# Performance work log

Measured on AMD Instinct MI355X. Metric: run time of the kernel, lower is better.

## Reference

```python
import jax, jax.numpy as jnp
import numpy as np

T, D, H = 2048, 2048, 16
C = D // H  # head dim = 128

def setup_inputs() -> dict:
    key = jax.random.key(0)
    k1, k2, k3 = jax.random.split(key, 3)
    x = jax.random.normal(k1, (T, D), dtype=jnp.float32)
    W_attn = jax.random.normal(k2, (3 * D, D), dtype=jnp.float32) * 0.02
    W_proj = jax.random.normal(k3, (D, D), dtype=jnp.float32) * 0.02
    return {"x": x, "W_attn": W_attn, "W_proj": W_proj}

def reference(x, W_attn, W_proj):
    # c_attn: per-token Linear -> [T, 3D]
    qkv = x @ W_attn.T
    q, k, v = jnp.split(qkv, 3, axis=-1)  # each [T, D]
    # [T, D] -> [H, T, C]
    q = q.reshape(T, H, C).transpose(1, 0, 2)
    k = k.reshape(T, H, C).transpose(1, 0, 2)
    v = v.reshape(T, H, C).transpose(1, 0, 2)
    # raw scores [H, T, T]
    scores = jnp.einsum('htc,hsc->hts', q, k)
    causal_mask = jnp.tril(jnp.ones((1, T, T))) == 0
    scores = jnp.where(causal_mask, float('-inf'), scores)
    orig_dtype = scores.dtype
    # NOTE: original scales AFTER masking, inside softmax, in fp32
    attn = jax.nn.softmax(scores.astype(jnp.float32) / jnp.sqrt(jnp.float32(C)), axis=-1)
    attn = attn.astype(orig_dtype)
    out = attn @ v  # [H, T, C]
    out = out.transpose(1, 0, 2).reshape(T, D)
    return out @ W_proj.T
```

## Files before the change

### kernel.cpp

```cpp
#include <hip/hip_runtime.h>
#include <hip/hip_bf16.h>
#include <stdint.h>

typedef __attribute__((ext_vector_type(8))) __bf16 bf16x8;
typedef __attribute__((ext_vector_type(4))) float f32x4;
typedef __attribute__((ext_vector_type(4))) unsigned int u32x4;
typedef __attribute__((ext_vector_type(4))) unsigned short u16x4;

__device__ __forceinline__ unsigned short f2bf(float f) {
  union { float f; unsigned int u; } v; v.f = f;
  unsigned int r = v.u + 0x7fffu + ((v.u >> 16) & 1u);
  return (unsigned short)(r >> 16);
}

__device__ __forceinline__ void gload_lds16(const void* g, void* l) {
  __builtin_amdgcn_global_load_lds(
      (const __attribute__((address_space(1))) unsigned int*)g,
      (__attribute__((address_space(3))) unsigned int*)l, 16, 0, 0);
}

__global__ __launch_bounds__(256) void cast_f32_bf16(const float* __restrict__ in,
                                                     unsigned short* __restrict__ out,
                                                     int n) {
  int i = (blockIdx.x * 256 + threadIdx.x) * 4;
  if (i >= n) return;
  f32x4 v = *(const f32x4*)&in[i];
  u16x4 o;
  o[0] = f2bf(v[0]); o[1] = f2bf(v[1]); o[2] = f2bf(v[2]); o[3] = f2bf(v[3]);
  *(u16x4*)&out[i] = o;
}

__global__ __launch_bounds__(256) void addf32(float* __restrict__ out,
                                              const float* __restrict__ part, int n) {
  int i = (blockIdx.x * 256 + threadIdx.x) * 4;
  if (i >= n) return;
  f32x4 a = *(const f32x4*)&out[i];
  f32x4 b = *(const f32x4*)&part[i];
  a[0] += b[0]; a[1] += b[1]; a[2] += b[2]; a[3] += b[3];
  *(f32x4*)&out[i] = a;
}

template<int OUT_BF16>
__global__ __launch_bounds__(256) void gemm_bt(const unsigned short* __restrict__ A,
                                               const unsigned short* __restrict__ B,
                                               void* __restrict__ Cv,
                                               float* __restrict__ Cp,
                                               int M, int N, int K, int KS) {
  __shared__ unsigned short As[2][128 * 32];
  __shared__ unsigned short Bs[2][128 * 32];

  const int tid  = threadIdx.x;
  const int lane = tid & 63;
  const int wave = tid >> 6;
  const int wr = (wave >> 1) * 64;
  const int wc = (wave & 1) * 64;
  const int row0 = blockIdx.y * 128;
  const int col0 = blockIdx.x * 128;
  const int l16 = lane & 15;
  const int lk  = (lane >> 4) * 8;
  const int kbeg = blockIdx.z * KS;

  const int srow = lane >> 2;
  const int sc   = (lane & 3) * 8;

  f32x4 acc[4][4] = {};

#pragma unroll
  for (int i = 0; i < 2; ++i) {
    int t = wave * 2 + i;
    int r = t * 16 + srow;
    gload_lds16(&A[(size_t)(row0 + r) * K + kbeg + sc], &As[0][t * 512]);
    gload_lds16(&B[(size_t)(col0 + r) * K + kbeg + sc], &Bs[0][t * 512]);
  }
  __syncthreads();

  int cur = 0;
  for (int k0 = kbeg; k0 < kbeg + KS; k0 += 32, cur ^= 1) {
    if (k0 + 32 < kbeg + KS) {
#pragma unroll
      for (int i = 0; i < 2; ++i) {
        int t = wave * 2 + i;
        int r = t * 16 + srow;
        gload_lds16(&A[(size_t)(row0 + r) * K + k0 + 32 + sc], &As[cur ^ 1][t * 512]);
        gload_lds16(&B[(size_t)(col0 + r) * K + k0 + 32 + sc], &Bs[cur ^ 1][t * 512]);
      }
    }

    bf16x8 af[4], bfr[4];
#pragma unroll
    for (int i = 0; i < 4; ++i) af[i]  = *(const bf16x8*)&As[cur][(wr + i * 16 + l16) * 32 + lk];
#pragma unroll
    for (int i = 0; i < 4; ++i) bfr[i] = *(const bf16x8*)&Bs[cur][(wc + i * 16 + l16) * 32 + lk];
#pragma unroll
    for (int i = 0; i < 4; ++i)
#pragma unroll
      for (int j = 0; j < 4; ++j)
        acc[i][j] = __builtin_amdgcn_mfma_f32_16x16x32_bf16(af[i], bfr[j], acc[i][j], 0, 0, 0);

    __syncthreads();
  }

  void* outp = (blockIdx.z == 0) ? Cv : (void*)Cp;

  const int orow = (lane >> 4) * 4;
#pragma unroll
  for (int i = 0; i < 4; ++i)
#pragma unroll
    for (int j = 0; j < 4; ++j)
#pragma unroll
      for (int r = 0; r < 4; ++r) {
        size_t gr = row0 + wr + i * 16 + orow + r;
        size_t gc = col0 + wc + j * 16 + l16;
        float v = acc[i][j][r];
        if (OUT_BF16) ((unsigned short*)outp)[gr * N + gc] = f2bf(v);
        else          ((float*)outp)[gr * N + gc] = v;
      }
}

#define KS_IDX(r, c) ((((r) * 128) + (c)) ^ (((r) & 7) << 3))
#define VT_IDX(c, t) ((((c) * 64) + (t)) ^ (((((c) ^ ((c) >> 3))) & 7) << 3))
#define PS_IDX(q, c) ((((q) * 64) + (c)) ^ (((((q) & 7) ^ (((q) >> 2) & 3))) << 3))

__global__ __launch_bounds__(256, 2) void attn_kernel(const unsigned short* __restrict__ qkv,
                                                      unsigned short* __restrict__ ctx) {
  __shared__ unsigned short Ks[2][64 * 128];
  __shared__ unsigned short VTs[2][128 * 64];
  __shared__ unsigned short Ps[4][16 * 64];

  const int tid  = threadIdx.x;
  const int lane = tid & 63;
  const int w    = tid >> 6;
  const int l16  = lane & 15;
  const int lk8  = (lane >> 4) * 8;

  const int flat = blockIdx.x + blockIdx.y * 32;
  int h, qb;
  if (flat < 256) { h = flat >> 5; qb = flat & 31; }
  else            { int f2 = flat - 256; h = 8 + (f2 >> 5); qb = 31 - (f2 & 31); }

  const int qrow = qb * 64 + w * 16;

  const unsigned short* Kbase = qkv + 2048 + h * 128;
  const unsigned short* Vbase = qkv + 4096 + h * 128;

  bf16x8 qf[4];
#pragma unroll
  for (int kk = 0; kk < 4; ++kk)
    qf[kk] = *(const bf16x8*)&qkv[(size_t)(qrow + l16) * 6144 + h * 128 + kk * 32 + lk8];

  f32x4 o[8] = {};
  float m[4], ls[4];
#pragma unroll
  for (int r = 0; r < 4; ++r) { m[r] = -1e30f; ls[r] = 0.f; }

  const float sscale = 0.08838834764831845f * 1.4426950408889634f;
  const int qg0 = qrow + (lane >> 4) * 4;

  const int t0v = (tid & 15) * 4;
  const int c0v = (tid >> 4) * 8;

  {
    u32x4 kr[4], vr[4];
#pragma unroll
    for (int it = 0; it < 4; ++it) {
      int idx = it * 256 + tid;
      int row = idx >> 4, c0 = (idx & 15) * 8;
      kr[it] = *(const u32x4*)&Kbase[(size_t)row * 6144 + c0];
    }
#pragma unroll
    for (int r = 0; r < 4; ++r)
      vr[r] = *(const u32x4*)&Vbase[(size_t)(t0v + r) * 6144 + c0v];
#pragma unroll
    for (int it = 0; it < 4; ++it) {
      int idx = it * 256 + tid;
      int row = idx >> 4, c0 = (idx & 15) * 8;
      *(u32x4*)&Ks[0][KS_IDX(row, c0)] = kr[it];
    }
    const unsigned short* p0 = (const unsigned short*)&vr[0];
    const unsigned short* p1 = (const unsigned short*)&vr[1];
    const unsigned short* p2 = (const unsigned short*)&vr[2];
    const unsigned short* p3 = (const unsigned short*)&vr[3];
#pragma unroll
    for (int j = 0; j < 8; ++j) {
      u16x4 wv; wv[0] = p0[j]; wv[1] = p1[j]; wv[2] = p2[j]; wv[3] = p3[j];
      *(u16x4*)&VTs[0][VT_IDX(c0v + j, t0v)] = wv;
    }
  }

  const int nkb = qb + 1;
  for (int kb = 0; kb < nkb; ++kb) {
    const int cur = kb & 1;
    const bool pre = (kb + 1 < nkb);

    u32x4 kr[4], vr[4];
    if (pre) {
#pragma unroll
      for (int it = 0; it < 4; ++it) {
        int idx = it * 256 + tid;
        int row = idx >> 4, c0 = (idx & 15) * 8;
        kr[it] = *(const u32x4*)&Kbase[(size_t)((kb + 1) * 64 + row) * 6144 + c0];
      }
#pragma unroll
      for (int r = 0; r < 4; ++r)
        vr[r] = *(const u32x4*)&Vbase[(size_t)((kb + 1) * 64 + t0v + r) * 6144 + c0v];
    }

    __syncthreads();

    if (pre) {
#pragma unroll
      for (int it = 0; it < 4; ++it) {
        int idx = it * 256 + tid;
        int row = idx >> 4, c0 = (idx & 15) * 8;
        *(u32x4*)&Ks[cur ^ 1][KS_IDX(row, c0)] = kr[it];
      }
      const unsigned short* p0 = (const unsigned short*)&vr[0];
      const unsigned short* p1 = (const unsigned short*)&vr[1];
      const unsigned short* p2 = (const unsigned short*)&vr[2];
      const unsigned short* p3 = (const unsigned short*)&vr[3];
#pragma unroll
      for (int j = 0; j < 8; ++j) {
        u16x4 wv; wv[0] = p0[j]; wv[1] = p1[j]; wv[2] = p2[j]; wv[3] = p3[j];
        *(u16x4*)&VTs[cur ^ 1][VT_IDX(c0v + j, t0v)] = wv;
      }
    }

    f32x4 s[4] = {};
#pragma unroll
    for (int n = 0; n < 4; ++n)
#pragma unroll
      for (int kk = 0; kk < 4; ++kk) {
        bf16x8 kf = *(const bf16x8*)&Ks[cur][KS_IDX(n * 16 + l16, kk * 32 + lk8)];
        s[n] = __builtin_amdgcn_mfma_f32_16x16x32_bf16(qf[kk], kf, s[n], 0, 0, 0);
      }

    const bool diag = (kb == qb);
    float pmax[4];
#pragma unroll
    for (int r = 0; r < 4; ++r) pmax[r] = -1e30f;
#pragma unroll
    for (int n = 0; n < 4; ++n) {
      int kg = kb * 64 + n * 16 + l16;
#pragma unroll
      for (int r = 0; r < 4; ++r) {
        float v = s[n][r] * sscale;
        if (diag && kg > qg0 + r) v = -1e30f;
        s[n][r] = v;
        pmax[r] = fmaxf(pmax[r], v);
      }
    }

    bool need = (pmax[0] > m[0] + 8.f) | (pmax[1] > m[1] + 8.f) |
                (pmax[2] > m[2] + 8.f) | (pmax[3] > m[3] + 8.f);
    if (__ballot(need)) {
#pragma unroll
      for (int d = 1; d < 16; d <<= 1)
#pragma unroll
        for (int r = 0; r < 4; ++r) pmax[r] = fmaxf(pmax[r], __shfl_xor(pmax[r], d));
#pragma unroll
      for (int r = 0; r < 4; ++r) {
        float mn = fmaxf(m[r], pmax[r]);
        float alpha = exp2f(m[r] - mn);
        m[r] = mn;
        ls[r] *= alpha;
#pragma unroll
        for (int n = 0; n < 8; ++n) o[n][r] *= alpha;
      }
    }

#pragma unroll
    for (int n = 0; n < 4; ++n)
#pragma unroll
      for (int r = 0; r < 4; ++r) {
        float p = exp2f(s[n][r] - m[r]);
        ls[r] += p;
        Ps[w][PS_IDX((lane >> 4) * 4 + r, n * 16 + l16)] = f2bf(p);
      }
    asm volatile("s_waitcnt lgkmcnt(0)" ::: "memory");

#pragma unroll
    for (int kk = 0; kk < 2; ++kk) {
      bf16x8 pf = *(const bf16x8*)&Ps[w][PS_IDX(l16, kk * 32 + lk8)];
#pragma unroll
      for (int n = 0; n < 8; ++n) {
        bf16x8 vf = *(const bf16x8*)&VTs[cur][VT_IDX(n * 16 + l16, kk * 32 + lk8)];
        o[n] = __builtin_amdgcn_mfma_f32_16x16x32_bf16(pf, vf, o[n], 0, 0, 0);
      }
    }
  }

#pragma unroll
  for (int d = 1; d < 16; d <<= 1)
#pragma unroll
    for (int r = 0; r < 4; ++r) ls[r] += __shfl_xor(ls[r], d);

#pragma unroll
  for (int r = 0; r < 4; ++r) {
    float inv = 1.0f / ls[r];
    size_t gr = qrow + (lane >> 4) * 4 + r;
#pragma unroll
    for (int n = 0; n < 8; ++n)
      ctx[gr * 2048 + h * 128 + n * 16 + l16] = f2bf(o[n][r] * inv);
  }
}

extern "C" void kernel_launch(void* const* d_in, const int* in_sizes, int n_in,
                              void* d_out, int out_size, void* d_ws, size_t ws_size,
                              hipStream_t stream) {
  const float* x  = (const float*)d_in[0];
  const float* Wa = (const float*)d_in[1];
  const float* Wp = (const float*)d_in[2];
  float* out = (float*)d_out;

  char* ws = (char*)d_ws;
  unsigned short* xb   = (unsigned short*)(ws);
  unsigned short* wab  = (unsigned short*)(ws + 8388608);
  unsigned short* wpb  = (unsigned short*)(ws + 33554432);
  unsigned short* qkvb = (unsigned short*)(ws + 41943040);
  unsigned short* ctx  = (unsigned short*)(ws + 67108864);
  float* proj_part     = (float*)(ws + 75497472);
  const bool splitk = ws_size >= (size_t)(75497472 + 16777216);

  cast_f32_bf16<<<4096, 256, 0, stream>>>(x, xb, 2048 * 2048);
  cast_f32_bf16<<<12288, 256, 0, stream>>>(Wa, wab, 6144 * 2048);
  cast_f32_bf16<<<4096, 256, 0, stream>>>(Wp, wpb, 2048 * 2048);

  gemm_bt<1><<<dim3(48, 16, 1), 256, 0, stream>>>(xb, wab, qkvb, nullptr,
                                                  2048, 6144, 2048, 2048);

  attn_kernel<<<dim3(32, 16), 256, 0, stream>>>(qkvb, ctx);

  if (splitk) {
    gemm_bt<0><<<dim3(16, 16, 2), 256, 0, stream>>>(ctx, wpb, out, proj_part,
                                                    2048, 2048, 2048, 1024);
    addf32<<<4096, 256, 0, stream>>>(out, proj_part, 2048 * 2048);
  } else {
    gemm_bt<0><<<dim3(16, 16, 1), 256, 0, stream>>>(ctx, wpb, out, nullptr,
                                                    2048, 2048, 2048, 2048);
  }
}
```

Baseline: 278.5 us.

## Swizzle GEMM LDS layout and use three-way split-K for projection

Applies an XOR swizzle to the LDS tile layout in the bf16 GEMM so fragment reads from shared memory hit fewer bank conflicts. Changes the output projection from two-way to three-way split-K with a clamped last chunk, reusing dead workspace regions for the partial sums and summing both partials in one reduction kernel. This raises the block count for better CU occupancy, at the cost of one extra partial buffer write and read.

```diff
diff --git a/kernel.cpp b/kernel.cpp
--- a/kernel.cpp
+++ b/kernel.cpp
@@ -30,13 +30,16 @@
   *(u16x4*)&out[i] = o;
 }
 
-__global__ __launch_bounds__(256) void addf32(float* __restrict__ out,
-                                              const float* __restrict__ part, int n) {
+__global__ __launch_bounds__(256) void add2f32(float* __restrict__ out,
+                                               const float* __restrict__ p1,
+                                               const float* __restrict__ p2, int n) {
   int i = (blockIdx.x * 256 + threadIdx.x) * 4;
   if (i >= n) return;
   f32x4 a = *(const f32x4*)&out[i];
-  f32x4 b = *(const f32x4*)&part[i];
-  a[0] += b[0]; a[1] += b[1]; a[2] += b[2]; a[3] += b[3];
+  f32x4 b = *(const f32x4*)&p1[i];
+  f32x4 c = *(const f32x4*)&p2[i];
+  a[0] += b[0] + c[0]; a[1] += b[1] + c[1];
+  a[2] += b[2] + c[2]; a[3] += b[3] + c[3];
   *(f32x4*)&out[i] = a;
 }
 
@@ -44,7 +47,8 @@
 __global__ __launch_bounds__(256) void gemm_bt(const unsigned short* __restrict__ A,
                                                const unsigned short* __restrict__ B,
                                                void* __restrict__ Cv,
-                                               float* __restrict__ Cp,
+                                               float* __restrict__ Cp1,
+                                               float* __restrict__ Cp2,
                                                int M, int N, int K, int KS) {
   __shared__ unsigned short As[2][128 * 32];
   __shared__ unsigned short Bs[2][128 * 32];
@@ -57,11 +61,12 @@
   const int row0 = blockIdx.y * 128;
   const int col0 = blockIdx.x * 128;
   const int l16 = lane & 15;
-  const int lk  = (lane >> 4) * 8;
+  const int lkA = ((lane >> 4) ^ (lane & 3)) * 8;
   const int kbeg = blockIdx.z * KS;
+  const int kend = (kbeg + KS < K) ? (kbeg + KS) : K;
 
   const int srow = lane >> 2;
-  const int sc   = (lane & 3) * 8;
+  const int scs  = ((lane & 3) ^ ((lane >> 2) & 3)) * 8;
 
   f32x4 acc[4][4] = {};
 
@@ -69,28 +74,28 @@
   for (int i = 0; i < 2; ++i) {
     int t = wave * 2 + i;
     int r = t * 16 + srow;
-    gload_lds16(&A[(size_t)(row0 + r) * K + kbeg + sc], &As[0][t * 512]);
-    gload_lds16(&B[(size_t)(col0 + r) * K + kbeg + sc], &Bs[0][t * 512]);
+    gload_lds16(&A[(size_t)(row0 + r) * K + kbeg + scs], &As[0][t * 512]);
+    gload_lds16(&B[(size_t)(col0 + r) * K + kbeg + scs], &Bs[0][t * 512]);
   }
   __syncthreads();
 
   int cur = 0;
-  for (int k0 = kbeg; k0 < kbeg + KS; k0 += 32, cur ^= 1) {
-    if (k0 + 32 < kbeg + KS) {
+  for (int k0 = kbeg; k0 < kend; k0 += 32, cur ^= 1) {
+    if (k0 + 32 < kend) {
 #pragma unroll
       for (int i = 0; i < 2; ++i) {
         int t = wave * 2 + i;
         int r = t * 16 + srow;
-        gload_lds16(&A[(size_t)(row0 + r) * K + k0 + 32 + sc], &As[cur ^ 1][t * 512]);
-        gload_lds16(&B[(size_t)(col0 + r) * K + k0 + 32 + sc], &Bs[cur ^ 1][t * 512]);
+        gload_lds16(&A[(size_t)(row0 + r) * K + k0 + 32 + scs], &As[cur ^ 1][t * 512]);
+        gload_lds16(&B[(size_t)(col0 + r) * K + k0 + 32 + scs], &Bs[cur ^ 1][t * 512]);
       }
     }
 
     bf16x8 af[4], bfr[4];
 #pragma unroll
-    for (int i = 0; i < 4; ++i) af[i]  = *(const bf16x8*)&As[cur][(wr + i * 16 + l16) * 32 + lk];
-#pragma unroll
-    for (int i = 0; i < 4; ++i) bfr[i] = *(const bf16x8*)&Bs[cur][(wc + i * 16 + l16) * 32 + lk];
+    for (int i = 0; i < 4; ++i) af[i]  = *(const bf16x8*)&As[cur][(wr + i * 16 + l16) * 32 + lkA];
+#pragma unroll
+    for (int i = 0; i < 4; ++i) bfr[i] = *(const bf16x8*)&Bs[cur][(wc + i * 16 + l16) * 32 + lkA];
 #pragma unroll
     for (int i = 0; i < 4; ++i)
 #pragma unroll
@@ -100,7 +105,7 @@
     __syncthreads();
   }
 
-  void* outp = (blockIdx.z == 0) ? Cv : (void*)Cp;
+  void* outp = (blockIdx.z == 0) ? Cv : (blockIdx.z == 1 ? (void*)Cp1 : (void*)Cp2);
 
   const int orow = (lane >> 4) * 4;
 #pragma unroll
@@ -318,24 +323,19 @@
   unsigned short* wpb  = (unsigned short*)(ws + 33554432);
   unsigned short* qkvb = (unsigned short*)(ws + 41943040);
   unsigned short* ctx  = (unsigned short*)(ws + 67108864);
-  float* proj_part     = (float*)(ws + 75497472);
-  const bool splitk = ws_size >= (size_t)(75497472 + 16777216);
+  float* proj_p1 = (float*)(ws + 8388608);
+  float* proj_p2 = (float*)(ws + 41943040);
 
   cast_f32_bf16<<<4096, 256, 0, stream>>>(x, xb, 2048 * 2048);
   cast_f32_bf16<<<12288, 256, 0, stream>>>(Wa, wab, 6144 * 2048);
   cast_f32_bf16<<<4096, 256, 0, stream>>>(Wp, wpb, 2048 * 2048);
 
-  gemm_bt<1><<<dim3(48, 16, 1), 256, 0, stream>>>(xb, wab, qkvb, nullptr,
+  gemm_bt<1><<<dim3(48, 16, 1), 256, 0, stream>>>(xb, wab, qkvb, nullptr, nullptr,
                                                   2048, 6144, 2048, 2048);
 
   attn_kernel<<<dim3(32, 16), 256, 0, stream>>>(qkvb, ctx);
 
-  if (splitk) {
-    gemm_bt<0><<<dim3(16, 16, 2), 256, 0, stream>>>(ctx, wpb, out, proj_part,
-                                                    2048, 2048, 2048, 1024);
-    addf32<<<4096, 256, 0, stream>>>(out, proj_part, 2048 * 2048);
-  } else {
-    gemm_bt<0><<<dim3(16, 16, 1), 256, 0, stream>>>(ctx, wpb, out, nullptr,
-                                                    2048, 2048, 2048, 2048);
-  }
-}
+  gemm_bt<0><<<dim3(16, 16, 3), 256, 0, stream>>>(ctx, wpb, out, proj_p1, proj_p2,
+                                                  2048, 2048, 2048, 704);
+  add2f32<<<4096, 256, 0, stream>>>(out, proj_p1, proj_p2, 2048 * 2048);
+}
```

After: 277.9 us. Within noise of the previous version (-0.2%).
